# Optimization experiments

Measured on AMD Instinct MI355X. Metric: run time of the kernel, lower is better.

The kernel has to match this reference:

```python
import jax, jax.numpy as jnp
import numpy as np

B, L, D_IN, H = 16, 2048, 1024, 512  # bidirectional: out_size = 2*H = D_IN (k=3 SRU layout)


def setup_inputs() -> dict:
    key = jax.random.key(0)
    k1, k2, k3, k4 = jax.random.split(key, 4)
    x = jax.random.normal(k1, (B, L, D_IN), dtype=jnp.float32)
    W = jax.random.normal(k2, (D_IN, 2, H, 3), dtype=jnp.float32) * 0.02
    bf = jax.random.normal(k3, (2, H), dtype=jnp.float32) * 0.02
    br = jax.random.normal(k4, (2, H), dtype=jnp.float32) * 0.02
    return {"x": x, "W": W, "bf": bf, "br": br}


def _sru_scan(xtil, f, r, xres, reverse):
    # xtil/f/r/xres: (L, B, H). Diagonal linear recurrence:
    #   c_t = f_t * c_{t-1} + (1 - f_t) * xtil_t
    #   h_t = r_t * tanh(c_t) + (1 - r_t) * xres_t
    def step(c, inp):
        xt_, f_, r_, xr_ = inp
        c = f_ * c + (1.0 - f_) * xt_
        h = r_ * jnp.tanh(c) + (1.0 - r_) * xr_
        return c, h
    c0 = jnp.zeros(xtil.shape[1:], dtype=xtil.dtype)
    c_last, h = jax.lax.scan(step, c0, (xtil, f, r, xres), reverse=reverse)
    return h, c_last


def reference(x, W, bf, br):
    xt = jnp.transpose(x, (1, 0, 2))  # (L, B, D_IN), as the wrapper does x.transpose(0,1)
    # U: (L, B, 2 dirs, H, 3 = [x_tilde, f_pre, r_pre])
    U = jnp.einsum("lbi,idhk->lbdhk", xt, W)
    f = jax.nn.sigmoid(U[..., 1] + bf[None, None, :, :])  # (L,B,2,H)
    r = jax.nn.sigmoid(U[..., 2] + br[None, None, :, :])
    xtil = U[..., 0]
    # highway/residual: raw input split per direction since n_in == 2*H (k=3)
    xres = xt.reshape(L, B, 2, H)

    h_f, c_f = _sru_scan(xtil[:, :, 0], f[:, :, 0], r[:, :, 0], xres[:, :, 0], reverse=False)
    h_b, c_b = _sru_scan(xtil[:, :, 1], f[:, :, 1], r[:, :, 1], xres[:, :, 1], reverse=True)

    h = jnp.concatenate([h_f, h_b], axis=-1)          # (L, B, 2H)
    c = jnp.concatenate([c_f, c_b], axis=-1)          # (B, 2H) final cell states
    # wrapper returns (out.transpose(0,1), c.transpose(0,1))
    return jnp.transpose(h, (1, 0, 2)), c.T
```

## Files before the change

kernel.cpp:

```cpp
#include <hip/hip_runtime.h>
#include <stdint.h>

#define B_    16
#define L_    2048
#define DIN_  1024
#define H_    512
#define NCOL_ 3072
#define M_    (B_ * L_)
#define K_    DIN_
#define NCHUNK 16
#define CHUNK  128

typedef unsigned short u16;
typedef __bf16 bf16_t;
typedef bf16_t bf16x8 __attribute__((ext_vector_type(8)));
typedef float  f32x4  __attribute__((ext_vector_type(4)));

__device__ __forceinline__ u16 f2bf(float f) {
  union { float f; uint32_t u; } v; v.f = f;
  return (u16)((v.u + 0x7fffu + ((v.u >> 16) & 1u)) >> 16);
}
__device__ __forceinline__ float bf2f(u16 b) {
  union { uint32_t u; float f; } v; v.u = ((uint32_t)b) << 16; return v.f;
}
__device__ __forceinline__ u16 f2h(float f) {
  _Float16 h = (_Float16)f; return *(u16*)&h;
}
__device__ __forceinline__ float h2f(u16 b) {
  _Float16 h = *(_Float16*)&b; return (float)h;
}

__global__ void cvt_x_kernel(const float4* __restrict__ x, ushort4* __restrict__ xb) {
  int i = blockIdx.x * blockDim.x + threadIdx.x;
  float4 v = x[i];
  ushort4 o;
  o.x = f2bf(v.x); o.y = f2bf(v.y); o.z = f2bf(v.z); o.w = f2bf(v.w);
  xb[i] = o;
}

__global__ void transpose_w_kernel(const float* __restrict__ W, u16* __restrict__ Wt) {
  __shared__ float s[32][33];
  int n0 = blockIdx.x * 32;
  int i0 = blockIdx.y * 32;
  int tx = threadIdx.x, ty = threadIdx.y;
  #pragma unroll
  for (int y = 0; y < 32; y += 8)
    s[ty + y][tx] = W[(uint64_t)(i0 + ty + y) * NCOL_ + n0 + tx];
  __syncthreads();
  #pragma unroll
  for (int y = 0; y < 32; y += 8) {
    int n = n0 + ty + y;
    int kk = n % 3, d = n / 1536, h = (n % 1536) / 3;
    int np = kk * 1024 + d * 512 + h;
    Wt[(uint64_t)np * K_ + i0 + tx] = f2bf(s[tx][ty + y]);
  }
}

__device__ __forceinline__ void gload_lds16(const void* g, void* lds) {
  __builtin_amdgcn_global_load_lds(
      (const __attribute__((address_space(1))) uint32_t*)g,
      (__attribute__((address_space(3))) uint32_t*)lds, 16, 0, 0);
}

__device__ __forceinline__ bf16x8 lds_rd(const u16* lds, int byteOff) {
  return __builtin_bit_cast(bf16x8, *(const f32x4*)((const char*)lds + byteOff));
}

__global__ __launch_bounds__(512, 2) void gemm_u_kernel(const u16* __restrict__ A,
                                                        const u16* __restrict__ Bt,
                                                        const float* __restrict__ bfp,
                                                        const float* __restrict__ brp,
                                                        u16* __restrict__ xtilP,
                                                        u16* __restrict__ fP,
                                                        u16* __restrict__ rP) {
  __shared__ __align__(16) u16 lds[81920];

  const int bid = blockIdx.x;
  const int xcd = bid & 7;
  const int li  = bid >> 3;
  const int bm  = xcd * 16 + (li & 15);
  const int bn  = li >> 4;
  const int m0 = bm * 256, n0 = bn * 256;

  const int tid  = threadIdx.x;
  const int w    = tid >> 6, lane = tid & 63;
  const int wr   = w >> 2, wc = w & 3;
  const int rr   = lane & 15, hs = lane >> 4;
  const int swzRd = (rr & 7) << 4;
  const int hsOff = hs * 16;

  const int rStage = w * 8 + (lane >> 3);
  const int sCol   = ((lane & 7) ^ ((lane >> 3) & 7)) * 8;
  const int ldsChunk = w * 1024;

  f32x4 acc[8][4] = {};

  auto stageA = [&](int bufBase, int kt) {
    #pragma unroll
    for (int h = 0; h < 2; ++h)
      #pragma unroll
      for (int j = 0; j < 2; ++j)
        gload_lds16(A + (uint64_t)(m0 + h * 128 + j * 64 + rStage) * K_ + kt + sCol,
                    (char*)lds + bufBase + h * 16384 + j * 8192 + ldsChunk);
  };
  auto stageB = [&](int bufBase, int kt) {
    #pragma unroll
    for (int h = 0; h < 2; ++h)
      #pragma unroll
      for (int j = 0; j < 2; ++j)
        gload_lds16(Bt + (uint64_t)(n0 + h * 128 + j * 64 + rStage) * K_ + kt + sCol,
                    (char*)lds + bufBase + h * 16384 + j * 8192 + ldsChunk);
  };

  stageA(0, 0);
  stageB(65536, 0);
  stageB(65536 + 32768, 64);
  asm volatile("s_waitcnt vmcnt(4)" ::: "memory");
  __builtin_amdgcn_sched_barrier(0);
  __builtin_amdgcn_s_barrier();

  const int aHalfBase = wr * 16384;
  const int bQuart    = (wc >> 1) * 16384;
  const int rowB0     = (wc & 1) * 64;

  int b3 = 0;
  #pragma unroll 1
  for (int t = 0; t < 16; ++t) {
    const int curA = (t & 1) << 15;
    const int curB = 65536 + b3 * 32768;
    const int b3n2 = (b3 >= 1) ? (b3 - 1) : 2;

    if (t < 15) stageA((~t & 1) << 15, (t + 1) * 64);
    if (t < 14) stageB(65536 + b3n2 * 32768, (t + 2) * 64);

    bf16x8 bF[4][2];
    #pragma unroll
    for (int ni = 0; ni < 4; ++ni)
      #pragma unroll
      for (int ks = 0; ks < 2; ++ks)
        bF[ni][ks] = lds_rd(lds, curB + bQuart + (rowB0 + ni * 16 + rr) * 128 + ((ks * 64 + hsOff) ^ swzRd));

    #pragma unroll
    for (int q = 0; q < 4; ++q) {
      bf16x8 a0[2], a1[2];
      #pragma unroll
      for (int ks = 0; ks < 2; ++ks) {
        a0[ks] = lds_rd(lds, curA + aHalfBase + ((2 * q) * 16 + rr) * 128 + ((ks * 64 + hsOff) ^ swzRd));
        a1[ks] = lds_rd(lds, curA + aHalfBase + ((2 * q + 1) * 16 + rr) * 128 + ((ks * 64 + hsOff) ^ swzRd));
      }
      #pragma unroll
      for (int ni = 0; ni < 4; ++ni)
        #pragma unroll
        for (int ks = 0; ks < 2; ++ks) {
          acc[2 * q][ni]     = __builtin_amdgcn_mfma_f32_16x16x32_bf16(a0[ks], bF[ni][ks], acc[2 * q][ni], 0, 0, 0);
          acc[2 * q + 1][ni] = __builtin_amdgcn_mfma_f32_16x16x32_bf16(a1[ks], bF[ni][ks], acc[2 * q + 1][ni], 0, 0, 0);
        }
    }

    if (t < 14) {
      asm volatile("s_waitcnt vmcnt(4)" ::: "memory");
      __builtin_amdgcn_sched_barrier(0);
    } else if (t == 14) {
      asm volatile("s_waitcnt vmcnt(0)" ::: "memory");
      __builtin_amdgcn_sched_barrier(0);
    }
    if (t < 15) __builtin_amdgcn_s_barrier();

    b3 = (b3 + 1 == 3) ? 0 : b3 + 1;
  }

  const int kkPlane = n0 >> 10;
  const int chBase  = n0 & 1023;
  u16* plane = (kkPlane == 0) ? xtilP : (kkPlane == 1 ? fP : rP);
  const float* biasp = (kkPlane == 1) ? bfp : brp;
  #pragma unroll
  for (int mi = 0; mi < 8; ++mi) {
    #pragma unroll
    for (int ni = 0; ni < 4; ++ni) {
      const int ch = chBase + wc * 64 + ni * 16 + rr;
      const float bias = kkPlane ? biasp[ch] : 0.f;
      #pragma unroll
      for (int i = 0; i < 4; ++i) {
        const int row = m0 + wr * 128 + mi * 16 + hs * 4 + i;
        float v = acc[mi][ni][i];
        if (kkPlane) v = 1.f / (1.f + __expf(-(v + bias)));
        plane[(uint64_t)row * 1024 + ch] = f2h(v);
      }
    }
  }
}

__global__ __launch_bounds__(256) void scan_partial_kernel(const u16* __restrict__ xtilP,
                                                           const u16* __restrict__ fP,
                                                           float* __restrict__ cpart,
                                                           float* __restrict__ Pp) {
  int tid = blockIdx.x * 256 + threadIdx.x;
  int ch = tid & 1023, chunk = (tid >> 10) & (NCHUNK - 1), b = tid >> 14;
  int d = ch >> 9;
  int l = chunk * CHUNK + (d ? CHUNK - 1 : 0);
  int64_t stride = d ? -1024 : 1024;
  uint64_t base = ((uint64_t)b * L_ + l) * 1024 + ch;
  float c = 0.f, P = 1.f;
  #pragma unroll 4
  for (int it = 0; it < CHUNK; ++it) {
    float f  = h2f(fP[base]);
    float xt = h2f(xtilP[base]);
    c = f * c + (1.f - f) * xt;
    P *= f;
    base += stride;
  }
  int o = (b * NCHUNK + chunk) * 1024 + ch;
  cpart[o] = c;
  Pp[o] = P;
}

__global__ void scan_combine_kernel(const float* __restrict__ cpart, const float* __restrict__ Pp,
                                    float* __restrict__ cin, float* __restrict__ outc) {
  int tid = blockIdx.x * blockDim.x + threadIdx.x;
  int ch = tid & 1023, b = tid >> 10, d = ch >> 9;
  float c = 0.f;
  for (int i = 0; i < NCHUNK; ++i) {
    int chunk = d ? (NCHUNK - 1 - i) : i;
    int o = (b * NCHUNK + chunk) * 1024 + ch;
    cin[o] = c;
    c = cpart[o] + Pp[o] * c;
  }
  outc[ch * B_ + b] = c;
}

__global__ __launch_bounds__(256) void scan_final_kernel(const u16* __restrict__ xb,
                                                         const u16* __restrict__ xtilP,
                                                         const u16* __restrict__ fP,
                                                         const u16* __restrict__ rP,
                                                         const float* __restrict__ cin,
                                                         float* __restrict__ outh) {
  int tid = blockIdx.x * 256 + threadIdx.x;
  int ch = tid & 1023, chunk = (tid >> 10) & (NCHUNK - 1), b = tid >> 14;
  int d = ch >> 9;
  int l = chunk * CHUNK + (d ? CHUNK - 1 : 0);
  int64_t stride = d ? -1024 : 1024;
  uint64_t base = ((uint64_t)b * L_ + l) * 1024 + ch;
  float c = cin[(b * NCHUNK + chunk) * 1024 + ch];
  #pragma unroll 2
  for (int it = 0; it < CHUNK; ++it) {
    float f    = h2f(fP[base]);
    float xt   = h2f(xtilP[base]);
    float rr   = h2f(rP[base]);
    float xres = bf2f(xb[base]);
    c = f * c + (1.f - f) * xt;
    float th = 1.f - 2.f / (__expf(2.f * c) + 1.f);
    outh[base] = rr * th + (1.f - rr) * xres;
    base += stride;
  }
}

extern "C" void kernel_launch(void* const* d_in, const int* in_sizes, int n_in,
                              void* d_out, int out_size, void* d_ws, size_t ws_size,
                              hipStream_t stream) {
  const float* x   = (const float*)d_in[0];
  const float* W   = (const float*)d_in[1];
  const float* bfp = (const float*)d_in[2];
  const float* brp = (const float*)d_in[3];

  float* outh = (float*)d_out;
  float* outc = outh + (size_t)B_ * L_ * DIN_;

  u16* xb = (u16*)d_ws;
  u16* Wt = xb + (size_t)M_ * K_;
  u16* xtilP = Wt + (size_t)NCOL_ * K_;
  u16* fP    = xtilP + (size_t)M_ * 1024;
  u16* rP    = fP    + (size_t)M_ * 1024;
  float* cpart = (float*)Wt;
  float* Pp    = cpart + (size_t)B_ * NCHUNK * 1024;
  float* cin   = Pp    + (size_t)B_ * NCHUNK * 1024;

  cvt_x_kernel<<<(M_ * K_ / 4) / 256, 256, 0, stream>>>((const float4*)x, (ushort4*)xb);
  transpose_w_kernel<<<dim3(NCOL_ / 32, K_ / 32), dim3(32, 8), 0, stream>>>(W, Wt);
  gemm_u_kernel<<<(M_ / 256) * (NCOL_ / 256), 512, 0, stream>>>(xb, Wt, bfp, brp, xtilP, fP, rP);
  scan_partial_kernel<<<(B_ * NCHUNK * 1024) / 256, 256, 0, stream>>>(xtilP, fP, cpart, Pp);
  scan_combine_kernel<<<(B_ * 2 * H_) / 256, 256, 0, stream>>>(cpart, Pp, cin, outc);
  scan_final_kernel<<<(B_ * NCHUNK * 1024) / 256, 256, 0, stream>>>(xb, xtilP, fP, rP, cin, outh);
}
```

Measured before the change: 381.0 us.

## Interleave global-to-LDS staging with MFMA phases and swap A/B buffering roles

Restructures the GEMM main loop so that A, rather than B, is triple-buffered and B is double-buffered. Global-to-LDS loads are split into halves and issued across the four q sub-phases, with barriers and s_setprio raising priority around each MFMA block. The aim is to spread memory traffic evenly and overlap it with matrix math in a ping-pong style schedule. In exchange it adds several more workgroup barriers per k-step, which could stall if the waves are not balanced.

```diff
diff --git a/kernel.cpp b/kernel.cpp
--- a/kernel.cpp
+++ b/kernel.cpp
@@ -95,50 +95,44 @@
 
   f32x4 acc[8][4] = {};
 
-  auto stageA = [&](int bufBase, int kt) {
-    #pragma unroll
-    for (int h = 0; h < 2; ++h)
-      #pragma unroll
-      for (int j = 0; j < 2; ++j)
-        gload_lds16(A + (uint64_t)(m0 + h * 128 + j * 64 + rStage) * K_ + kt + sCol,
-                    (char*)lds + bufBase + h * 16384 + j * 8192 + ldsChunk);
+  auto stageAh = [&](int bufBase, int kt, int part) {
+    #pragma unroll
+    for (int u = 0; u < 2; ++u) {
+      const int hh = part * 2 + u, h = hh >> 1, j = hh & 1;
+      gload_lds16(A + (uint64_t)(m0 + h * 128 + j * 64 + rStage) * K_ + kt + sCol,
+                  (char*)lds + bufBase + h * 16384 + j * 8192 + ldsChunk);
+    }
   };
-  auto stageB = [&](int bufBase, int kt) {
-    #pragma unroll
-    for (int h = 0; h < 2; ++h)
-      #pragma unroll
-      for (int j = 0; j < 2; ++j)
-        gload_lds16(Bt + (uint64_t)(n0 + h * 128 + j * 64 + rStage) * K_ + kt + sCol,
-                    (char*)lds + bufBase + h * 16384 + j * 8192 + ldsChunk);
+  auto stageBh = [&](int bufBase, int kt, int part) {
+    #pragma unroll
+    for (int u = 0; u < 2; ++u) {
+      const int hh = part * 2 + u, h = hh >> 1, j = hh & 1;
+      gload_lds16(Bt + (uint64_t)(n0 + h * 128 + j * 64 + rStage) * K_ + kt + sCol,
+                  (char*)lds + bufBase + h * 16384 + j * 8192 + ldsChunk);
+    }
   };
 
-  stageA(0, 0);
-  stageB(65536, 0);
-  stageB(65536 + 32768, 64);
+  stageBh(98304, 0, 0); stageBh(98304, 0, 1);
+  stageAh(0, 0, 0);     stageAh(0, 0, 1);
+  stageAh(32768, 64, 0); stageAh(32768, 64, 1);
   asm volatile("s_waitcnt vmcnt(4)" ::: "memory");
   __builtin_amdgcn_sched_barrier(0);
   __builtin_amdgcn_s_barrier();
 
   const int aHalfBase = wr * 16384;
-  const int bQuart    = (wc >> 1) * 16384;
+  const int bHalfBase = (wc >> 1) * 16384;
   const int rowB0     = (wc & 1) * 64;
 
-  int b3 = 0;
+  int a3 = 0;
   #pragma unroll 1
   for (int t = 0; t < 16; ++t) {
-    const int curA = (t & 1) << 15;
-    const int curB = 65536 + b3 * 32768;
-    const int b3n2 = (b3 >= 1) ? (b3 - 1) : 2;
-
-    if (t < 15) stageA((~t & 1) << 15, (t + 1) * 64);
-    if (t < 14) stageB(65536 + b3n2 * 32768, (t + 2) * 64);
+    const int curA = a3 * 32768;
+    const int curB = 98304 + (t & 1) * 32768;
+    const int nxtB = 98304 + ((t + 1) & 1) * 32768;
+    const int a3n2 = (a3 >= 1) ? (a3 - 1) : 2;
+    const int nxtA = a3n2 * 32768;
 
     bf16x8 bF[4][2];
-    #pragma unroll
-    for (int ni = 0; ni < 4; ++ni)
-      #pragma unroll
-      for (int ks = 0; ks < 2; ++ks)
-        bF[ni][ks] = lds_rd(lds, curB + bQuart + (rowB0 + ni * 16 + rr) * 128 + ((ks * 64 + hsOff) ^ swzRd));
 
     #pragma unroll
     for (int q = 0; q < 4; ++q) {
@@ -148,6 +142,23 @@
         a0[ks] = lds_rd(lds, curA + aHalfBase + ((2 * q) * 16 + rr) * 128 + ((ks * 64 + hsOff) ^ swzRd));
         a1[ks] = lds_rd(lds, curA + aHalfBase + ((2 * q + 1) * 16 + rr) * 128 + ((ks * 64 + hsOff) ^ swzRd));
       }
+      if (q == 0) {
+        #pragma unroll
+        for (int ni = 0; ni < 4; ++ni)
+          #pragma unroll
+          for (int ks = 0; ks < 2; ++ks)
+            bF[ni][ks] = lds_rd(lds, curB + bHalfBase + (rowB0 + ni * 16 + rr) * 128 + ((ks * 64 + hsOff) ^ swzRd));
+      }
+      if (q == 0 && t < 15) stageBh(nxtB, (t + 1) * 64, 0);
+      if (q == 1 && t < 15) stageBh(nxtB, (t + 1) * 64, 1);
+      if (q == 2 && t < 14) stageAh(nxtA, (t + 2) * 64, 0);
+      if (q == 3 && t < 14) stageAh(nxtA, (t + 2) * 64, 1);
+
+      __builtin_amdgcn_sched_barrier(0);
+      __builtin_amdgcn_s_barrier();
+      asm volatile("s_waitcnt lgkmcnt(0)" ::: "memory");
+      __builtin_amdgcn_sched_barrier(0);
+      __builtin_amdgcn_s_setprio(1);
       #pragma unroll
       for (int ni = 0; ni < 4; ++ni)
         #pragma unroll
@@ -155,18 +166,20 @@
           acc[2 * q][ni]     = __builtin_amdgcn_mfma_f32_16x16x32_bf16(a0[ks], bF[ni][ks], acc[2 * q][ni], 0, 0, 0);
           acc[2 * q + 1][ni] = __builtin_amdgcn_mfma_f32_16x16x32_bf16(a1[ks], bF[ni][ks], acc[2 * q + 1][ni], 0, 0, 0);
         }
-    }
-
-    if (t < 14) {
-      asm volatile("s_waitcnt vmcnt(4)" ::: "memory");
-      __builtin_amdgcn_sched_barrier(0);
-    } else if (t == 14) {
-      asm volatile("s_waitcnt vmcnt(0)" ::: "memory");
-      __builtin_amdgcn_sched_barrier(0);
-    }
-    if (t < 15) __builtin_amdgcn_s_barrier();
-
-    b3 = (b3 + 1 == 3) ? 0 : b3 + 1;
+      __builtin_amdgcn_s_setprio(0);
+      if (q == 3) {
+        if (t < 14) {
+          asm volatile("s_waitcnt vmcnt(4)" ::: "memory");
+          __builtin_amdgcn_sched_barrier(0);
+        } else if (t == 14) {
+          asm volatile("s_waitcnt vmcnt(0)" ::: "memory");
+          __builtin_amdgcn_sched_barrier(0);
+        }
+      }
+      __builtin_amdgcn_s_barrier();
+    }
+
+    a3 = (a3 + 1 == 3) ? 0 : a3 + 1;
   }
 
   const int kkPlane = n0 >> 10;
```

Result: no change. 386.6 us (+1.5%).
